# Kernel tuning notes

Hardware: AMD Instinct MI355X
Metric: run time of the kernel (lower is better)

The kernel has to match this reference:

```python
import jax, jax.numpy as jnp
import numpy as np

N = 102400          # total nodes (256 graphs x 400 nodes)
E = 3276800         # edges (avg degree 32)
B = 256             # num graphs
NODE_DIM, MRI_DIM, COG_DIM, CLIN_DIM, GEN_DIM, NUM_CLASSES = 128, 256, 64, 32, 512, 3
EPS = 1e-5

def _lin(k, i, o):
    kw, kb = jax.random.split(k)
    s = 1.0 / np.sqrt(i)
    return (jax.random.uniform(kw, (i, o), jnp.float32, -s, s),
            jax.random.uniform(kb, (o,), jnp.float32, -s, s))

def setup_inputs() -> dict:
    key = jax.random.key(0)
    ks = jax.random.split(key, 20)
    inp = {}
    inp['x'] = jax.random.normal(ks[0], (N, NODE_DIM), jnp.float32)
    inp['edge_index'] = jax.random.randint(ks[1], (2, E), 0, N)
    inp['batch'] = jnp.repeat(jnp.arange(B, dtype=jnp.int32), N // B)
    inp['mri'] = jax.random.normal(ks[2], (B, MRI_DIM), jnp.float32)
    inp['cog'] = jax.random.normal(ks[3], (B, COG_DIM), jnp.float32)
    inp['clin'] = jax.random.normal(ks[4], (B, CLIN_DIM), jnp.float32)
    inp['gen'] = jax.random.normal(ks[5], (B, GEN_DIM), jnp.float32)
    inp['W1'], inp['b1'] = _lin(ks[6], NODE_DIM, 64)
    inp['W2'], inp['b2'] = _lin(ks[7], 64, 32)
    inp['W3'], inp['b3'] = _lin(ks[8], 32, 16)
    inp['bn1_g'] = jnp.ones((64,), jnp.float32); inp['bn1_b'] = jnp.zeros((64,), jnp.float32)
    inp['bn2_g'] = jnp.ones((32,), jnp.float32); inp['bn2_b'] = jnp.zeros((32,), jnp.float32)
    inp['mriW'], inp['mrib'] = _lin(ks[9], MRI_DIM, 16)
    inp['cogW'], inp['cogb'] = _lin(ks[10], COG_DIM, 16)
    inp['clinW'], inp['clinb'] = _lin(ks[11], CLIN_DIM, 16)
    inp['genW'], inp['genb'] = _lin(ks[12], GEN_DIM, 16)
    inp['c1W'], inp['c1b'] = _lin(ks[13], 96, 64)  # 32 (pooled) + 64 (multimodal)
    inp['cbn1_g'] = jnp.ones((64,), jnp.float32); inp['cbn1_b'] = jnp.zeros((64,), jnp.float32)
    inp['c2W'], inp['c2b'] = _lin(ks[14], 64, 32)
    inp['cbn2_g'] = jnp.ones((32,), jnp.float32); inp['cbn2_b'] = jnp.zeros((32,), jnp.float32)
    inp['c3W'], inp['c3b'] = _lin(ks[15], 32, NUM_CLASSES)
    return inp

def _bn(h, g, b):
    # BatchNorm1d in training mode: biased batch stats
    m = h.mean(0)
    v = jnp.mean((h - m) ** 2, 0)
    return (h - m) * jax.lax.rsqrt(v + EPS) * g + b

def _gcn(h, W, bias, s, d, norm):
    # GCNConv: linear -> symmetric-normalized scatter-add aggregation (self-loops in s/d)
    h = h @ W
    agg = jnp.zeros_like(h).at[d].add(h[s] * norm[:, None])
    return agg + bias

def reference(x, edge_index, batch, mri, cog, clin, gen,
              W1, b1, W2, b2, W3, b3, bn1_g, bn1_b, bn2_g, bn2_b,
              mriW, mrib, cogW, cogb, clinW, clinb, genW, genb,
              c1W, c1b, cbn1_g, cbn1_b, c2W, c2b, cbn2_g, cbn2_b, c3W, c3b):
    n = x.shape[0]
    loop = jnp.arange(n)
    s = jnp.concatenate([edge_index[0], loop])
    d = jnp.concatenate([edge_index[1], loop])
    deg = jnp.zeros((n,), x.dtype).at[d].add(1.0)
    dinv = jax.lax.rsqrt(deg)  # deg >= 1 due to self-loops
    norm = dinv[s] * dinv[d]

    x1 = jax.nn.relu(_bn(_gcn(x, W1, b1, s, d, norm), bn1_g, bn1_b))
    x2 = jax.nn.relu(_bn(_gcn(x1, W2, b2, s, d, norm), bn2_g, bn2_b))
    gf = jax.nn.relu(_gcn(x2, W3, b3, s, d, norm))  # [N,16]

    cnt = jax.ops.segment_sum(jnp.ones((n,), x.dtype), batch, num_segments=B)
    g_mean = jax.ops.segment_sum(gf, batch, num_segments=B) / cnt[:, None]
    g_max = jax.ops.segment_max(gf, batch, num_segments=B)
    g_emb = jnp.concatenate([g_mean, g_max], axis=1)  # [B,32]

    mm = jnp.concatenate([
        jax.nn.relu(mri @ mriW + mrib),
        jax.nn.relu(cog @ cogW + cogb),
        jax.nn.relu(clin @ clinW + clinb),
        jax.nn.relu(gen @ genW + genb)], axis=1)  # [B,64]

    h = jnp.concatenate([g_emb, mm], axis=1)  # [B,96]
    h = jax.nn.relu(_bn(h @ c1W + c1b, cbn1_g, cbn1_b))  # dropout = identity (eval)
    h = jax.nn.relu(_bn(h @ c2W + c2b, cbn2_g, cbn2_b))
    out = h @ c3W + c3b
    return jax.nn.log_softmax(out, axis=1)
```

## Files before the change

### kernel.cpp

```cpp
#include <hip/hip_runtime.h>
#include <hip/hip_bf16.h>

#define TPB 256
#define BSHIFT 9
#define BNODES 512
#define CH 4096

typedef unsigned long long u64;
typedef __attribute__((ext_vector_type(8))) short short8;
typedef __attribute__((ext_vector_type(4))) float f32x4;

__device__ inline unsigned short f2bf(float f) {
    unsigned u = __float_as_uint(f);
    return (unsigned short)((u + 0x7FFF + ((u >> 16) & 1)) >> 16);
}
__device__ inline float bf2f(short s) {
    return __uint_as_float(((unsigned)(unsigned short)s) << 16);
}


__global__ void k_bhist(const int* __restrict__ dstp, int* __restrict__ bcnt, int E, int nbuk) {
    __shared__ int h[256];
    int tid = threadIdx.x;
    h[tid] = 0;
    __syncthreads();
    int e0 = blockIdx.x * CH;
    int e1 = min(e0 + CH, E);
    for (int e = e0 + tid; e < e1; e += TPB) atomicAdd(&h[dstp[e] >> BSHIFT], 1);
    __syncthreads();
    if (tid < nbuk && h[tid]) atomicAdd(&bcnt[tid], h[tid]);
}

__global__ void k_bscan(const int* __restrict__ bcnt, int* __restrict__ bbase,
                        int* __restrict__ gcur, int nbuk, int E) {
    __shared__ int s[256];
    int tid = threadIdx.x;
    int v = (tid < nbuk) ? bcnt[tid] : 0;
    s[tid] = v;
    __syncthreads();
    for (int o = 1; o < 256; o <<= 1) {
        int t = (tid >= o) ? s[tid - o] : 0;
        __syncthreads();
        s[tid] += t;
        __syncthreads();
    }
    if (tid < nbuk) { int e = s[tid] - v; bbase[tid] = e; gcur[tid] = e; }
    if (tid == 0) bbase[nbuk] = E;
}

__global__ void k_partition(const int* __restrict__ ei, int* __restrict__ gcur,
                            u64* __restrict__ part, int E, int nbuk) {
    __shared__ int h[256], baseg[256], scn[256], cur[256];
    __shared__ u64 stage[CH];
    int tid = threadIdx.x;
    h[tid] = 0;
    __syncthreads();
    int e0 = blockIdx.x * CH;
    int ecnt = min(CH, E - e0);
    const int* srcp = ei;
    const int* dstp = ei + E;
    for (int i = tid; i < ecnt; i += TPB) atomicAdd(&h[dstp[e0 + i] >> BSHIFT], 1);
    __syncthreads();
    int v = h[tid];
    if (tid < nbuk && v) baseg[tid] = atomicAdd(&gcur[tid], v);
    scn[tid] = v;
    __syncthreads();
    for (int o = 1; o < 256; o <<= 1) {
        int t = (tid >= o) ? scn[tid - o] : 0;
        __syncthreads();
        scn[tid] += t;
        __syncthreads();
    }
    int excl = scn[tid] - v;
    __syncthreads();
    scn[tid] = excl; cur[tid] = excl;
    __syncthreads();
    for (int i = tid; i < ecnt; i += TPB) {
        int s = srcp[e0 + i], d = dstp[e0 + i];
        int bk = d >> BSHIFT;
        int p = atomicAdd(&cur[bk], 1);
        stage[p] = ((u64)(unsigned)d << 32) | (unsigned)s;
    }
    __syncthreads();
    for (int i = tid; i < ecnt; i += TPB) {
        u64 vv = stage[i];
        int bk = (int)(vv >> 32) >> BSHIFT;
        part[baseg[bk] + (i - scn[bk])] = vv;
    }
}

__global__ void k_bucket_csr(const u64* __restrict__ part, const int* __restrict__ bbase,
                             float* __restrict__ dinv, int* __restrict__ offsets,
                             int* __restrict__ csr, int N, int nbuk) {
    __shared__ int cnt[BNODES];
    __shared__ int ps[256];
    __shared__ int off_s[BNODES];
    int b = blockIdx.x, tid = threadIdx.x;
    int n0 = b << BSHIFT;
    int nn = min(BNODES, N - n0);
    int j0 = bbase[b], j1 = bbase[b + 1];
    for (int i = tid; i < BNODES; i += TPB) cnt[i] = 0;
    __syncthreads();
    for (int j = j0 + tid; j < j1; j += TPB) {
        int dst = (int)(part[j] >> 32);
        atomicAdd(&cnt[dst - n0], 1);
    }
    __syncthreads();
    int a0 = cnt[2 * tid], a1 = cnt[2 * tid + 1];
    ps[tid] = a0 + a1;
    __syncthreads();
    for (int o = 1; o < 256; o <<= 1) {
        int t = (tid >= o) ? ps[tid - o] : 0;
        __syncthreads();
        ps[tid] += t;
        __syncthreads();
    }
    int excl = ps[tid] - (a0 + a1);
    off_s[2 * tid] = excl;
    off_s[2 * tid + 1] = excl + a0;
    __syncthreads();
    for (int i = tid; i < nn; i += TPB) {
        dinv[n0 + i] = rsqrtf((float)(cnt[i] + 1));
        offsets[n0 + i] = j0 + off_s[i];
    }
    if (b == nbuk - 1 && tid == 0) offsets[N] = j1;
    __syncthreads();
    for (int i = tid; i < BNODES; i += TPB) cnt[i] = j0 + off_s[i];
    __syncthreads();
    for (int j = j0 + tid; j < j1; j += TPB) {
        u64 vv = part[j];
        int dst = (int)(vv >> 32);
        int src = (int)(vv & 0xffffffffu);
        int pos = atomicAdd(&cnt[dst - n0], 1);
        csr[pos] = src;
    }
}


template<int K, bool BN, bool BF16IN>
__global__ void k_packA(const void* __restrict__ inv, const float* __restrict__ scale,
                        const float* __restrict__ shift, unsigned short* __restrict__ out) {
    constexpr int KB = K / 32;
    int g = blockIdx.x * TPB + threadIdx.x;
    int lane = g & 63, tile = g >> 6;
    int rowblk = tile / KB, kblk = tile - rowblk * KB;
    int row = rowblk * 16 + (lane & 15);
    int k0 = kblk * 32 + (lane >> 4) * 8;
    float vs[8];
    if (BF16IN) {
        const __hip_bfloat16* in = (const __hip_bfloat16*)inv;
        short8 sv = *reinterpret_cast<const short8*>(in + (size_t)row * K + k0);
        #pragma unroll
        for (int u = 0; u < 8; ++u) vs[u] = bf2f(sv[u]);
    } else {
        const float* in = (const float*)inv;
        const float4* p = reinterpret_cast<const float4*>(in + (size_t)row * K + k0);
        float4 v0 = p[0], v1 = p[1];
        vs[0] = v0.x; vs[1] = v0.y; vs[2] = v0.z; vs[3] = v0.w;
        vs[4] = v1.x; vs[5] = v1.y; vs[6] = v1.z; vs[7] = v1.w;
    }
    short8 rr;
    #pragma unroll
    for (int u = 0; u < 8; ++u) {
        float v = vs[u];
        if (BN) v = fmaxf(v * scale[k0 + u] + shift[k0 + u], 0.f);
        rr[u] = (short)f2bf(v);
    }
    *reinterpret_cast<short8*>(out + (size_t)g * 8) = rr;
}

__global__ void k_packW(const float* __restrict__ W1, const float* __restrict__ W2,
                        const float* __restrict__ W3, unsigned short* __restrict__ out) {
    int b = blockIdx.x, lane = threadIdx.x;
    const float* W; int KB, C; size_t off; int idx;
    if (b < 16)      { W = W1; KB = 4; C = 64; off = 0;     idx = b; }
    else if (b < 20) { W = W2; KB = 2; C = 32; off = 8192;  idx = b - 16; }
    else             { W = W3; KB = 1; C = 16; off = 10240; idx = b - 20; }
    int nblk = idx / KB, kblk = idx - nblk * KB;
    int col = nblk * 16 + (lane & 15);
    int k0 = kblk * 32 + (lane >> 4) * 8;
    short8 rr;
    #pragma unroll
    for (int j = 0; j < 8; ++j) rr[j] = (short)f2bf(W[(size_t)(k0 + j) * C + col]);
    *reinterpret_cast<short8*>(out + off + ((size_t)idx * 64 + lane) * 8) = rr;
}

template<int K, int C>
__global__ void k_mfma_gemm(const unsigned short* __restrict__ A,
                            const unsigned short* __restrict__ Wp,
                            const float* __restrict__ dinv,
                            __hip_bfloat16* __restrict__ hh, size_t slice) {
    constexpr int KB = K / 32, NB = C / 16;
    int lane = threadIdx.x & 63, w = threadIdx.x >> 6;
    int rowblk = blockIdx.x * 4 + w;
    const short8* Af = reinterpret_cast<const short8*>(A);
    const short8* Bf = reinterpret_cast<const short8*>(Wp);
    short8 b[NB][KB];
    #pragma unroll
    for (int nb = 0; nb < NB; ++nb)
        #pragma unroll
        for (int kb = 0; kb < KB; ++kb)
            b[nb][kb] = Bf[(nb * KB + kb) * 64 + lane];
    f32x4 z = {0.f, 0.f, 0.f, 0.f};
    f32x4 acc[NB];
    #pragma unroll
    for (int nb = 0; nb < NB; ++nb) acc[nb] = z;
    #pragma unroll
    for (int kb = 0; kb < KB; ++kb) {
        short8 a = Af[((size_t)rowblk * KB + kb) * 64 + lane];
        #pragma unroll
        for (int nb = 0; nb < NB; ++nb)
            acc[nb] = __builtin_amdgcn_mfma_f32_16x16x32_bf16(a, b[nb][kb], acc[nb], 0, 0, 0);
    }
    int colb = lane & 15;
    int node0 = rowblk * 16 + (lane >> 4) * 4;
    float dv[4];
    #pragma unroll
    for (int j = 0; j < 4; ++j) dv[j] = dinv[node0 + j];
    #pragma unroll
    for (int nb = 0; nb < NB; ++nb)
        #pragma unroll
        for (int j = 0; j < 4; ++j)
            hh[nb * slice + (size_t)(node0 + j) * 16 + colb] = __float2bfloat16(acc[nb][j] * dv[j]);
}

template<int CT, bool RELU, bool STATS>
__global__ void k_gather_row(const __hip_bfloat16* __restrict__ hhp,
                             const int* __restrict__ offs, const int* __restrict__ csr,
                             const float* __restrict__ dinv, const float* __restrict__ bias,
                             __hip_bfloat16* __restrict__ outp, float* __restrict__ pstat,
                             int n) {
    __shared__ float lred[16 * 272];
    __shared__ float sred[2 * 272];
    int tid = threadIdx.x;
    int g = tid >> 4, l = tid & 15;
    int node = blockIdx.x * 16 + g;
    int j0 = offs[node], j1 = offs[node + 1];
    float facc[16];
    #pragma unroll
    for (int u = 0; u < 16; ++u) facc[u] = 0.f;
    const short8* self = reinterpret_cast<const short8*>(hhp + (size_t)node * 16);
    if (l == 15) {
        short8 r0 = self[0], r1 = self[1];
        #pragma unroll
        for (int u = 0; u < 8; ++u) { facc[u] += bf2f(r0[u]); facc[8 + u] += bf2f(r1[u]); }
    }
    int j = j0 + l;
    for (; j + 16 < j1; j += 32) {
        int s0 = __builtin_nontemporal_load(&csr[j]);
        int s1 = __builtin_nontemporal_load(&csr[j + 16]);
        const short8* ra = reinterpret_cast<const short8*>(hhp + (size_t)s0 * 16);
        const short8* rb = reinterpret_cast<const short8*>(hhp + (size_t)s1 * 16);
        short8 a0 = ra[0], a1 = ra[1], b0 = rb[0], b1 = rb[1];
        #pragma unroll
        for (int u = 0; u < 8; ++u) {
            facc[u]     += bf2f(a0[u]) + bf2f(b0[u]);
            facc[8 + u] += bf2f(a1[u]) + bf2f(b1[u]);
        }
    }
    if (j < j1) {
        int s = __builtin_nontemporal_load(&csr[j]);
        const short8* row = reinterpret_cast<const short8*>(hhp + (size_t)s * 16);
        short8 r0 = row[0], r1 = row[1];
        #pragma unroll
        for (int u = 0; u < 8; ++u) { facc[u] += bf2f(r0[u]); facc[8 + u] += bf2f(r1[u]); }
    }
    int wbase = g * 272 + l * 17;
    #pragma unroll
    for (int u = 0; u < 16; ++u) lred[wbase + u] = facc[u];
    __syncthreads();
    int rbase = g * 272 + l;
    float acc = 0.f;
    #pragma unroll
    for (int k = 0; k < 16; ++k) acc += lred[rbase + k * 17];
    float v = dinv[node] * acc + bias[l];
    if (RELU) v = fmaxf(v, 0.f);
    outp[(size_t)node * CT + l] = __float2bfloat16(v);
    if (STATS) {
        sred[l * 17 + g] = v;
        sred[272 + l * 17 + g] = v * v;
        __syncthreads();
        if (tid < 32) {
            int c = tid & 15;
            const float* base = sred + (tid >> 4) * 272 + c * 17;
            float a = 0.f;
            #pragma unroll
            for (int k = 0; k < 16; ++k) a += base[k];
            pstat[(size_t)blockIdx.x * 32 + (tid >> 4) * 16 + c] = a;
        }
    }
}

__global__ void k_bnred(const float* __restrict__ pstat, float* __restrict__ bred, int G) {
    __shared__ float ss[256];
    int tid = threadIdx.x;
    int p = blockIdx.x >> 6, c = blockIdx.x & 63;
    int rows_per = (G + 63) >> 6;
    int r0 = c * rows_per, r1 = min(r0 + rows_per, G);
    const float* base = pstat + (size_t)p * G * 32;
    float acc = 0.f;
    for (int i = r0 * 32 + tid; i < r1 * 32; i += 256) acc += base[i];
    ss[tid] = acc;
    __syncthreads();
    #pragma unroll
    for (int o = 128; o >= 32; o >>= 1) {
        if (tid < o) ss[tid] += ss[tid + o];
        __syncthreads();
    }
    if (tid < 32) bred[(size_t)blockIdx.x * 32 + tid] = ss[tid];
}

__global__ void k_bnstat2(const float* __restrict__ bred, const float* __restrict__ g,
                          const float* __restrict__ b, float* __restrict__ scale,
                          float* __restrict__ shift, float invN) {
    __shared__ float ss[256];
    int tid = threadIdx.x, p = blockIdx.x;
    const float* base = bred + (size_t)p * 64 * 32;
    float acc = 0.f;
    for (int i = tid; i < 64 * 32; i += 256) acc += base[i];
    ss[tid] = acc;
    __syncthreads();
    #pragma unroll
    for (int o = 128; o >= 32; o >>= 1) {
        if (tid < o) ss[tid] += ss[tid + o];
        __syncthreads();
    }
    if (tid < 16) {
        int ch = p * 16 + tid;
        float m = ss[tid] * invN;
        float var = ss[16 + tid] * invN - m * m;
        float sc = g[ch] * rsqrtf(var + 1e-5f);
        scale[ch] = sc;
        shift[ch] = b[ch] - m * sc;
    }
}


__global__ void k_pool(const __hip_bfloat16* __restrict__ gf, float* __restrict__ h, int nper) {
    __shared__ float ssum[TPB], smax[TPB];
    int b = blockIdx.x, tid = threadIdx.x;
    int c = tid & 15, r0 = tid >> 4;
    const __hip_bfloat16* base = gf + (size_t)b * nper * 16;
    float s = 0.f, m = -1e30f;
    for (int r = r0; r < nper; r += 16) {
        float v = __bfloat162float(base[r * 16 + c]);
        s += v; m = fmaxf(m, v);
    }
    ssum[tid] = s; smax[tid] = m; __syncthreads();
    for (int off = 128; off >= 16; off >>= 1) {
        if (tid < off) { ssum[tid] += ssum[tid + off]; smax[tid] = fmaxf(smax[tid], smax[tid + off]); }
        __syncthreads();
    }
    if (tid < 16) { h[b * 96 + tid] = ssum[tid] / (float)nper; h[b * 96 + 16 + tid] = smax[tid]; }
}

__global__ void k_mm(const float* __restrict__ mri, const float* __restrict__ cog,
                     const float* __restrict__ clin, const float* __restrict__ gen,
                     const float* __restrict__ mriW, const float* __restrict__ mrib,
                     const float* __restrict__ cogW, const float* __restrict__ cogb,
                     const float* __restrict__ clinW, const float* __restrict__ clinb,
                     const float* __restrict__ genW, const float* __restrict__ genb,
                     float* __restrict__ h) {
    int b = blockIdx.x;
    int w = threadIdx.x >> 6;
    int lane = threadIdx.x & 63;
    int c = lane & 15, part = lane >> 4;
    const float* in; const float* W; const float* bias; int K;
    if (w == 0)      { in = mri  + b * 256; W = mriW;  bias = mrib;  K = 256; }
    else if (w == 1) { in = cog  + b * 64;  W = cogW;  bias = cogb;  K = 64;  }
    else if (w == 2) { in = clin + b * 32;  W = clinW; bias = clinb; K = 32;  }
    else             { in = gen  + b * 512; W = genW;  bias = genb;  K = 512; }
    int kq = K >> 2;
    int k0 = part * kq;
    float acc = 0.f;
    for (int k = k0; k < k0 + kq; k += 4) {
        float4 iv = *reinterpret_cast<const float4*>(in + k);
        acc += iv.x * W[k * 16 + c] + iv.y * W[(k + 1) * 16 + c]
             + iv.z * W[(k + 2) * 16 + c] + iv.w * W[(k + 3) * 16 + c];
    }
    acc += __shfl_xor(acc, 16);
    acc += __shfl_xor(acc, 32);
    if (part == 0) h[b * 96 + 32 + w * 16 + c] = fmaxf(acc + bias[c], 0.f);
}

__global__ void k_head1(const float* __restrict__ h, const float* __restrict__ W,
                        const float* __restrict__ bias, float* __restrict__ t1) {
    int gid = blockIdx.x * TPB + threadIdx.x;
    int b = gid >> 6, j = gid & 63;
    const float* hr = h + b * 96;
    float acc = bias[j];
    #pragma unroll
    for (int k = 0; k < 96; ++k) acc += hr[k] * W[k * 64 + j];
    t1[gid] = acc;
}

__global__ __launch_bounds__(1024) void k_headtail(
        float* __restrict__ t1g,
        const float* __restrict__ cbn1_g, const float* __restrict__ cbn1_b,
        const float* __restrict__ c2W, const float* __restrict__ c2b,
        const float* __restrict__ cbn2_g, const float* __restrict__ cbn2_b,
        const float* __restrict__ c3W, const float* __restrict__ c3b,
        float* __restrict__ out) {
    __shared__ float red[1024];
    __shared__ float t2s[256 * 32];
    __shared__ float sc1[64], sh1[64], sc2[32], sh2[32];
    int tid = threadIdx.x;
    const float invB = 1.0f / 256.0f;

    float psum = 0.f, psq = 0.f;
    for (int i = tid; i < 16384; i += 1024) {
        float v = t1g[i]; psum += v; psq += v * v;
    }
    red[tid] = psum; __syncthreads();
    for (int o = 512; o >= 64; o >>= 1) { if (tid < o) red[tid] += red[tid + o]; __syncthreads(); }
    if (tid < 64) sc1[tid] = red[tid];
    __syncthreads();
    red[tid] = psq; __syncthreads();
    for (int o = 512; o >= 64; o >>= 1) { if (tid < o) red[tid] += red[tid + o]; __syncthreads(); }
    if (tid < 64) {
        float m = sc1[tid] * invB;
        float var = red[tid] * invB - m * m;
        float s = cbn1_g[tid] * rsqrtf(var + 1e-5f);
        sc1[tid] = s; sh1[tid] = cbn1_b[tid] - m * s;
    }
    __syncthreads();
    for (int i = tid; i < 16384; i += 1024) {
        int k = i & 63;
        t1g[i] = fmaxf(t1g[i] * sc1[k] + sh1[k], 0.f);
    }
    __syncthreads();
    int j2 = tid & 31, g2 = tid >> 5;
    float p2 = 0.f, q2 = 0.f;
    for (int b = g2 * 8; b < g2 * 8 + 8; ++b) {
        const float* tr = t1g + b * 64;
        float acc = c2b[j2];
        #pragma unroll
        for (int k = 0; k < 64; ++k) acc += tr[k] * c2W[k * 32 + j2];
        t2s[b * 32 + j2] = acc; p2 += acc; q2 += acc * acc;
    }
    red[tid] = p2; __syncthreads();
    for (int o = 512; o >= 32; o >>= 1) { if (tid < o) red[tid] += red[tid + o]; __syncthreads(); }
    if (tid < 32) sc2[tid] = red[tid];
    __syncthreads();
    red[tid] = q2; __syncthreads();
    for (int o = 512; o >= 32; o >>= 1) { if (tid < o) red[tid] += red[tid + o]; __syncthreads(); }
    if (tid < 32) {
        float m = sc2[tid] * invB;
        float var = red[tid] * invB - m * m;
        float s = cbn2_g[tid] * rsqrtf(var + 1e-5f);
        sc2[tid] = s; sh2[tid] = cbn2_b[tid] - m * s;
    }
    __syncthreads();
    if (tid < 256) {
        const float* tr = t2s + tid * 32;
        float o0 = c3b[0], o1 = c3b[1], o2 = c3b[2];
        #pragma unroll
        for (int k = 0; k < 32; ++k) {
            float v = fmaxf(tr[k] * sc2[k] + sh2[k], 0.f);
            o0 += v * c3W[k * 3 + 0];
            o1 += v * c3W[k * 3 + 1];
            o2 += v * c3W[k * 3 + 2];
        }
        float m = fmaxf(fmaxf(o0, o1), o2);
        float lse = m + logf(expf(o0 - m) + expf(o1 - m) + expf(o2 - m));
        out[tid * 3 + 0] = o0 - lse;
        out[tid * 3 + 1] = o1 - lse;
        out[tid * 3 + 2] = o2 - lse;
    }
}


extern "C" void kernel_launch(void* const* d_in, const int* in_sizes, int n_in,
                              void* d_out, int out_size, void* d_ws, size_t ws_size,
                              hipStream_t stream) {
    const float* x    = (const float*)d_in[0];
    const int*   ei   = (const int*)d_in[1];
    const float* mri  = (const float*)d_in[3];
    const float* cog  = (const float*)d_in[4];
    const float* clin = (const float*)d_in[5];
    const float* gen  = (const float*)d_in[6];
    const float* W1 = (const float*)d_in[7];  const float* b1 = (const float*)d_in[8];
    const float* W2 = (const float*)d_in[9];  const float* b2 = (const float*)d_in[10];
    const float* W3 = (const float*)d_in[11]; const float* b3 = (const float*)d_in[12];
    const float* bn1_g = (const float*)d_in[13]; const float* bn1_b = (const float*)d_in[14];
    const float* bn2_g = (const float*)d_in[15]; const float* bn2_b = (const float*)d_in[16];
    const float* mriW = (const float*)d_in[17]; const float* mrib = (const float*)d_in[18];
    const float* cogW = (const float*)d_in[19]; const float* cogb = (const float*)d_in[20];
    const float* clinW = (const float*)d_in[21]; const float* clinb = (const float*)d_in[22];
    const float* genW = (const float*)d_in[23]; const float* genb = (const float*)d_in[24];
    const float* c1W = (const float*)d_in[25]; const float* c1b = (const float*)d_in[26];
    const float* cbn1_g = (const float*)d_in[27]; const float* cbn1_b = (const float*)d_in[28];
    const float* c2W = (const float*)d_in[29]; const float* c2b = (const float*)d_in[30];
    const float* cbn2_g = (const float*)d_in[31]; const float* cbn2_b = (const float*)d_in[32];
    const float* c3W = (const float*)d_in[33]; const float* c3b = (const float*)d_in[34];
    float* out = (float*)d_out;

    const int N = in_sizes[0] / 128;
    const int E = in_sizes[1] / 2;
    const int B = in_sizes[6] / 512;
    const int nper = N / B;
    const int nbuk = (N + BNODES - 1) >> BSHIFT;
    const int npart = (E + CH - 1) / CH;
    const int rowblks = N / 16;
    const int G = N / 16;

    char* ws = (char*)d_ws;
    size_t off = 0;
    auto alloc = [&](size_t bytes) -> void* {
        void* p = ws + off;
        off += (bytes + 255) & ~(size_t)255;
        return p;
    };
    int*   bcnt    = (int*)alloc(256 * 4);
    int*   bbase   = (int*)alloc((size_t)(nbuk + 1) * 4);
    int*   gcur    = (int*)alloc((size_t)nbuk * 4);
    u64*   part    = (u64*)alloc((size_t)E * 8);
    __hip_bfloat16* agg = (__hip_bfloat16*)part;
    int*   offsets = (int*)alloc((size_t)(N + 1) * 4);
    int*   csr     = (int*)alloc((size_t)E * 4);
    float* dinv    = (float*)alloc((size_t)N * 4);
    __hip_bfloat16* hh = (__hip_bfloat16*)alloc((size_t)N * 64 * 2);
    unsigned short* xb = (unsigned short*)alloc((size_t)N * 128 * 2);
    unsigned short* Wpack = (unsigned short*)alloc(10752 * 2);
    float* pstat   = (float*)alloc((size_t)6 * G * 32 * 4);
    float* bred    = (float*)alloc((size_t)6 * 64 * 32 * 4);
    float* scale1  = (float*)alloc(64 * 4);
    float* shift1  = (float*)alloc(64 * 4);
    float* scale2  = (float*)alloc(32 * 4);
    float* shift2  = (float*)alloc(32 * 4);
    float* hbuf    = (float*)alloc((size_t)B * 96 * 4);
    float* t1      = (float*)alloc((size_t)B * 64 * 4);
    (void)ws_size; (void)n_in; (void)out_size;

    hipMemsetAsync(bcnt, 0, 256 * 4, stream);

    k_bhist<<<npart, TPB, 0, stream>>>(ei + E, bcnt, E, nbuk);
    k_bscan<<<1, TPB, 0, stream>>>(bcnt, bbase, gcur, nbuk, E);
    k_partition<<<npart, TPB, 0, stream>>>(ei, gcur, part, E, nbuk);
    k_bucket_csr<<<nbuk, TPB, 0, stream>>>(part, bbase, dinv, offsets, csr, N, nbuk);
    k_packW<<<21, 64, 0, stream>>>(W1, W2, W3, Wpack);

    size_t slice = (size_t)N * 16;
    int gmm = rowblks / 4;

    k_packA<128, false, false><<<rowblks * 4 * 64 / TPB, TPB, 0, stream>>>(x, nullptr, nullptr, xb);
    k_mfma_gemm<128, 64><<<gmm, TPB, 0, stream>>>(xb, Wpack, dinv, hh, slice);
    for (int p = 0; p < 4; ++p)
        k_gather_row<64, false, true><<<G, TPB, 0, stream>>>(
            hh + p * slice, offsets, csr, dinv, b1 + p * 16,
            agg + p * 16, pstat + (size_t)p * G * 32, N);
    k_bnred<<<4 * 64, 256, 0, stream>>>(pstat, bred, G);
    k_bnstat2<<<4, 256, 0, stream>>>(bred, bn1_g, bn1_b, scale1, shift1, 1.0f / N);

    k_packA<64, true, true><<<rowblks * 2 * 64 / TPB, TPB, 0, stream>>>(agg, scale1, shift1, xb);
    k_mfma_gemm<64, 32><<<gmm, TPB, 0, stream>>>(xb, Wpack + 8192, dinv, hh, slice);
    for (int p = 0; p < 2; ++p)
        k_gather_row<32, false, true><<<G, TPB, 0, stream>>>(
            hh + p * slice, offsets, csr, dinv, b2 + p * 16,
            agg + p * 16, pstat + (size_t)(4 + p) * G * 32, N);
    k_bnred<<<2 * 64, 256, 0, stream>>>(pstat + (size_t)4 * G * 32, bred + 4 * 64 * 32, G);
    k_bnstat2<<<2, 256, 0, stream>>>(bred + 4 * 64 * 32, bn2_g, bn2_b, scale2, shift2, 1.0f / N);

    k_packA<32, true, true><<<rowblks * 1 * 64 / TPB, TPB, 0, stream>>>(agg, scale2, shift2, xb);
    k_mfma_gemm<32, 16><<<gmm, TPB, 0, stream>>>(xb, Wpack + 10240, dinv, hh, slice);
    k_gather_row<16, true, false><<<G, TPB, 0, stream>>>(hh, offsets, csr, dinv, b3, agg, nullptr, N);

    k_pool<<<B, TPB, 0, stream>>>(agg, hbuf, nper);
    k_mm<<<B, 256, 0, stream>>>(mri, cog, clin, gen, mriW, mrib, cogW, cogb,
                                clinW, clinb, genW, genb, hbuf);
    k_head1<<<(B * 64 + TPB - 1) / TPB, TPB, 0, stream>>>(hbuf, c1W, c1b, t1);
    k_headtail<<<1, 1024, 0, stream>>>(t1, cbn1_g, cbn1_b, c2W, c2b,
                                       cbn2_g, cbn2_b, c3W, c3b, out);
}
```

Baseline: 418.3 us.

## Gather 32-channel slices per pass to halve CSR traversals in GCN layers

The GEMM epilogue now writes features in 32-channel slices instead of 16, and a new gather kernel accumulates 32 channels per edge visit, so layer 1 takes two gather passes instead of four and layer 2 takes one instead of two. This cuts repeated reads of the CSR index array and the per-pass launch overhead, while each random row fetch becomes 64 bytes. The BN partial-stat reductions are resized to 64 entries per block, and the per-thread accumulator doubles to 32 floats, which raises register pressure. The bucket CSR build also switches its reads of the partitioned edge array to nontemporal loads.

New measurement: 408.1 us. -2.4%, faster.

```diff
diff --git a/kernel.cpp b/kernel.cpp
--- a/kernel.cpp
+++ b/kernel.cpp
@@ -102,8 +102,8 @@
     for (int i = tid; i < BNODES; i += TPB) cnt[i] = 0;
     __syncthreads();
     for (int j = j0 + tid; j < j1; j += TPB) {
-        int dst = (int)(part[j] >> 32);
-        atomicAdd(&cnt[dst - n0], 1);
+        u64 vv = __builtin_nontemporal_load(&part[j]);
+        atomicAdd(&cnt[(int)(vv >> 32) - n0], 1);
     }
     __syncthreads();
     int a0 = cnt[2 * tid], a1 = cnt[2 * tid + 1];
@@ -128,7 +128,7 @@
     for (int i = tid; i < BNODES; i += TPB) cnt[i] = j0 + off_s[i];
     __syncthreads();
     for (int j = j0 + tid; j < j1; j += TPB) {
-        u64 vv = part[j];
+        u64 vv = __builtin_nontemporal_load(&part[j]);
         int dst = (int)(vv >> 32);
         int src = (int)(vv & 0xffffffffu);
         int pos = atomicAdd(&cnt[dst - n0], 1);
@@ -185,7 +185,7 @@
     *reinterpret_cast<short8*>(out + off + ((size_t)idx * 64 + lane) * 8) = rr;
 }
 
-template<int K, int C>
+template<int K, int C, int SW>
 __global__ void k_mfma_gemm(const unsigned short* __restrict__ A,
                             const unsigned short* __restrict__ Wp,
                             const float* __restrict__ dinv,
@@ -218,20 +218,105 @@
     #pragma unroll
     for (int j = 0; j < 4; ++j) dv[j] = dinv[node0 + j];
     #pragma unroll
-    for (int nb = 0; nb < NB; ++nb)
+    for (int nb = 0; nb < NB; ++nb) {
+        int c = nb * 16 + colb;
+        size_t base = (size_t)(c / SW) * slice + (c % SW);
         #pragma unroll
         for (int j = 0; j < 4; ++j)
-            hh[nb * slice + (size_t)(node0 + j) * 16 + colb] = __float2bfloat16(acc[nb][j] * dv[j]);
+            hh[base + (size_t)(node0 + j) * SW] = __float2bfloat16(acc[nb][j] * dv[j]);
+    }
 }
 
 template<int CT, bool RELU, bool STATS>
+__global__ void k_gather_row32(const __hip_bfloat16* __restrict__ hhp,
+                               const int* __restrict__ offs, const int* __restrict__ csr,
+                               const float* __restrict__ dinv, const float* __restrict__ bias,
+                               __hip_bfloat16* __restrict__ outp, float* __restrict__ pstat,
+                               int n) {
+    __shared__ float lred[16 * 528];
+    __shared__ float sred[2 * 544];
+    int tid = threadIdx.x;
+    int g = tid >> 4, l = tid & 15;
+    int node = blockIdx.x * 16 + g;
+    int j0 = offs[node], j1 = offs[node + 1];
+    float facc[32];
+    #pragma unroll
+    for (int u = 0; u < 32; ++u) facc[u] = 0.f;
+    if (l == 15) {
+        const short8* sr = reinterpret_cast<const short8*>(hhp + (size_t)node * 32);
+        short8 r0 = sr[0], r1 = sr[1], r2 = sr[2], r3 = sr[3];
+        #pragma unroll
+        for (int u = 0; u < 8; ++u) {
+            facc[u] += bf2f(r0[u]);      facc[8 + u]  += bf2f(r1[u]);
+            facc[16 + u] += bf2f(r2[u]); facc[24 + u] += bf2f(r3[u]);
+        }
+    }
+    int j = j0 + l;
+    for (; j + 16 < j1; j += 32) {
+        int s0 = __builtin_nontemporal_load(&csr[j]);
+        int s1 = __builtin_nontemporal_load(&csr[j + 16]);
+        const short8* ra = reinterpret_cast<const short8*>(hhp + (size_t)s0 * 32);
+        const short8* rb = reinterpret_cast<const short8*>(hhp + (size_t)s1 * 32);
+        short8 a0 = ra[0], a1 = ra[1], a2 = ra[2], a3 = ra[3];
+        short8 b0 = rb[0], b1 = rb[1], b2 = rb[2], b3 = rb[3];
+        #pragma unroll
+        for (int u = 0; u < 8; ++u) {
+            facc[u]      += bf2f(a0[u]) + bf2f(b0[u]);
+            facc[8 + u]  += bf2f(a1[u]) + bf2f(b1[u]);
+            facc[16 + u] += bf2f(a2[u]) + bf2f(b2[u]);
+            facc[24 + u] += bf2f(a3[u]) + bf2f(b3[u]);
+        }
+    }
+    if (j < j1) {
+        int s = __builtin_nontemporal_load(&csr[j]);
+        const short8* rr = reinterpret_cast<const short8*>(hhp + (size_t)s * 32);
+        short8 r0 = rr[0], r1 = rr[1], r2 = rr[2], r3 = rr[3];
+        #pragma unroll
+        for (int u = 0; u < 8; ++u) {
+            facc[u] += bf2f(r0[u]);      facc[8 + u]  += bf2f(r1[u]);
+            facc[16 + u] += bf2f(r2[u]); facc[24 + u] += bf2f(r3[u]);
+        }
+    }
+    int wbase = g * 528 + l * 33;
+    #pragma unroll
+    for (int u = 0; u < 32; ++u) lred[wbase + u] = facc[u];
+    __syncthreads();
+    int rbase = g * 528 + l;
+    float alo = 0.f, ahi = 0.f;
+    #pragma unroll
+    for (int k = 0; k < 16; ++k) {
+        alo += lred[rbase + k * 33];
+        ahi += lred[rbase + k * 33 + 16];
+    }
+    float dv = dinv[node];
+    float vlo = dv * alo + bias[l];
+    float vhi = dv * ahi + bias[l + 16];
+    if (RELU) { vlo = fmaxf(vlo, 0.f); vhi = fmaxf(vhi, 0.f); }
+    outp[(size_t)node * CT + l]      = __float2bfloat16(vlo);
+    outp[(size_t)node * CT + l + 16] = __float2bfloat16(vhi);
+    if (STATS) {
+        sred[l * 17 + g]          = vlo;
+        sred[(l + 16) * 17 + g]   = vhi;
+        sred[544 + l * 17 + g]        = vlo * vlo;
+        sred[544 + (l + 16) * 17 + g] = vhi * vhi;
+        __syncthreads();
+        if (tid < 64) {
+            int which = tid >> 5, c = tid & 31;
+            const float* base = sred + which * 544 + c * 17;
+            float a = 0.f;
+            #pragma unroll
+            for (int k = 0; k < 16; ++k) a += base[k];
+            pstat[(size_t)blockIdx.x * 64 + which * 32 + c] = a;
+        }
+    }
+}
+
+template<int CT, bool RELU>
 __global__ void k_gather_row(const __hip_bfloat16* __restrict__ hhp,
                              const int* __restrict__ offs, const int* __restrict__ csr,
                              const float* __restrict__ dinv, const float* __restrict__ bias,
-                             __hip_bfloat16* __restrict__ outp, float* __restrict__ pstat,
-                             int n) {
+                             __hip_bfloat16* __restrict__ outp, int n) {
     __shared__ float lred[16 * 272];
-    __shared__ float sred[2 * 272];
     int tid = threadIdx.x;
     int g = tid >> 4, l = tid & 15;
     int node = blockIdx.x * 16 + g;
@@ -239,9 +324,9 @@
     float facc[16];
     #pragma unroll
     for (int u = 0; u < 16; ++u) facc[u] = 0.f;
-    const short8* self = reinterpret_cast<const short8*>(hhp + (size_t)node * 16);
     if (l == 15) {
-        short8 r0 = self[0], r1 = self[1];
+        const short8* sr = reinterpret_cast<const short8*>(hhp + (size_t)node * 16);
+        short8 r0 = sr[0], r1 = sr[1];
         #pragma unroll
         for (int u = 0; u < 8; ++u) { facc[u] += bf2f(r0[u]); facc[8 + u] += bf2f(r1[u]); }
     }
@@ -260,8 +345,8 @@
     }
     if (j < j1) {
         int s = __builtin_nontemporal_load(&csr[j]);
-        const short8* row = reinterpret_cast<const short8*>(hhp + (size_t)s * 16);
-        short8 r0 = row[0], r1 = row[1];
+        const short8* rr = reinterpret_cast<const short8*>(hhp + (size_t)s * 16);
+        short8 r0 = rr[0], r1 = rr[1];
         #pragma unroll
         for (int u = 0; u < 8; ++u) { facc[u] += bf2f(r0[u]); facc[8 + u] += bf2f(r1[u]); }
     }
@@ -276,19 +361,6 @@
     float v = dinv[node] * acc + bias[l];
     if (RELU) v = fmaxf(v, 0.f);
     outp[(size_t)node * CT + l] = __float2bfloat16(v);
-    if (STATS) {
-        sred[l * 17 + g] = v;
-        sred[272 + l * 17 + g] = v * v;
-        __syncthreads();
-        if (tid < 32) {
-            int c = tid & 15;
-            const float* base = sred + (tid >> 4) * 272 + c * 17;
-            float a = 0.f;
-            #pragma unroll
-            for (int k = 0; k < 16; ++k) a += base[k];
-            pstat[(size_t)blockIdx.x * 32 + (tid >> 4) * 16 + c] = a;
-        }
-    }
 }
 
 __global__ void k_bnred(const float* __restrict__ pstat, float* __restrict__ bred, int G) {
@@ -297,17 +369,17 @@
     int p = blockIdx.x >> 6, c = blockIdx.x & 63;
     int rows_per = (G + 63) >> 6;
     int r0 = c * rows_per, r1 = min(r0 + rows_per, G);
-    const float* base = pstat + (size_t)p * G * 32;
+    const float* base = pstat + (size_t)p * G * 64;
     float acc = 0.f;
-    for (int i = r0 * 32 + tid; i < r1 * 32; i += 256) acc += base[i];
+    for (int i = r0 * 64 + tid; i < r1 * 64; i += 256) acc += base[i];
     ss[tid] = acc;
     __syncthreads();
     #pragma unroll
-    for (int o = 128; o >= 32; o >>= 1) {
+    for (int o = 128; o >= 64; o >>= 1) {
         if (tid < o) ss[tid] += ss[tid + o];
         __syncthreads();
     }
-    if (tid < 32) bred[(size_t)blockIdx.x * 32 + tid] = ss[tid];
+    if (tid < 64) bred[(size_t)blockIdx.x * 64 + tid] = ss[tid];
 }
 
 __global__ void k_bnstat2(const float* __restrict__ bred, const float* __restrict__ g,
@@ -315,20 +387,20 @@
                           float* __restrict__ shift, float invN) {
     __shared__ float ss[256];
     int tid = threadIdx.x, p = blockIdx.x;
-    const float* base = bred + (size_t)p * 64 * 32;
+    const float* base = bred + (size_t)p * 64 * 64;
     float acc = 0.f;
-    for (int i = tid; i < 64 * 32; i += 256) acc += base[i];
+    for (int i = tid; i < 64 * 64; i += 256) acc += base[i];
     ss[tid] = acc;
     __syncthreads();
     #pragma unroll
-    for (int o = 128; o >= 32; o >>= 1) {
+    for (int o = 128; o >= 64; o >>= 1) {
         if (tid < o) ss[tid] += ss[tid + o];
         __syncthreads();
     }
-    if (tid < 16) {
-        int ch = p * 16 + tid;
+    if (tid < 32) {
+        int ch = p * 32 + tid;
         float m = ss[tid] * invN;
-        float var = ss[16 + tid] * invN - m * m;
+        float var = ss[32 + tid] * invN - m * m;
         float sc = g[ch] * rsqrtf(var + 1e-5f);
         scale[ch] = sc;
         shift[ch] = b[ch] - m * sc;
@@ -522,8 +594,8 @@
     __hip_bfloat16* hh = (__hip_bfloat16*)alloc((size_t)N * 64 * 2);
     unsigned short* xb = (unsigned short*)alloc((size_t)N * 128 * 2);
     unsigned short* Wpack = (unsigned short*)alloc(10752 * 2);
-    float* pstat   = (float*)alloc((size_t)6 * G * 32 * 4);
-    float* bred    = (float*)alloc((size_t)6 * 64 * 32 * 4);
+    float* pstat   = (float*)alloc((size_t)3 * G * 64 * 4);
+    float* bred    = (float*)alloc((size_t)3 * 64 * 64 * 4);
     float* scale1  = (float*)alloc(64 * 4);
     float* shift1  = (float*)alloc(64 * 4);
     float* scale2  = (float*)alloc(32 * 4);
@@ -540,30 +612,28 @@
     k_bucket_csr<<<nbuk, TPB, 0, stream>>>(part, bbase, dinv, offsets, csr, N, nbuk);
     k_packW<<<21, 64, 0, stream>>>(W1, W2, W3, Wpack);
 
-    size_t slice = (size_t)N * 16;
+    size_t slice32 = (size_t)N * 32;
     int gmm = rowblks / 4;
 
     k_packA<128, false, false><<<rowblks * 4 * 64 / TPB, TPB, 0, stream>>>(x, nullptr, nullptr, xb);
-    k_mfma_gemm<128, 64><<<gmm, TPB, 0, stream>>>(xb, Wpack, dinv, hh, slice);
-    for (int p = 0; p < 4; ++p)
-        k_gather_row<64, false, true><<<G, TPB, 0, stream>>>(
-            hh + p * slice, offsets, csr, dinv, b1 + p * 16,
-            agg + p * 16, pstat + (size_t)p * G * 32, N);
-    k_bnred<<<4 * 64, 256, 0, stream>>>(pstat, bred, G);
-    k_bnstat2<<<4, 256, 0, stream>>>(bred, bn1_g, bn1_b, scale1, shift1, 1.0f / N);
+    k_mfma_gemm<128, 64, 32><<<gmm, TPB, 0, stream>>>(xb, Wpack, dinv, hh, slice32);
+    for (int p = 0; p < 2; ++p)
+        k_gather_row32<64, false, true><<<G, TPB, 0, stream>>>(
+            hh + p * slice32, offsets, csr, dinv, b1 + p * 32,
+            agg + p * 32, pstat + (size_t)p * G * 64, N);
+    k_bnred<<<2 * 64, 256, 0, stream>>>(pstat, bred, G);
+    k_bnstat2<<<2, 256, 0, stream>>>(bred, bn1_g, bn1_b, scale1, shift1, 1.0f / N);
 
     k_packA<64, true, true><<<rowblks * 2 * 64 / TPB, TPB, 0, stream>>>(agg, scale1, shift1, xb);
-    k_mfma_gemm<64, 32><<<gmm, TPB, 0, stream>>>(xb, Wpack + 8192, dinv, hh, slice);
-    for (int p = 0; p < 2; ++p)
-        k_gather_row<32, false, true><<<G, TPB, 0, stream>>>(
-            hh + p * slice, offsets, csr, dinv, b2 + p * 16,
-            agg + p * 16, pstat + (size_t)(4 + p) * G * 32, N);
-    k_bnred<<<2 * 64, 256, 0, stream>>>(pstat + (size_t)4 * G * 32, bred + 4 * 64 * 32, G);
-    k_bnstat2<<<2, 256, 0, stream>>>(bred + 4 * 64 * 32, bn2_g, bn2_b, scale2, shift2, 1.0f / N);
+    k_mfma_gemm<64, 32, 32><<<gmm, TPB, 0, stream>>>(xb, Wpack + 8192, dinv, hh, slice32);
+    k_gather_row32<32, false, true><<<G, TPB, 0, stream>>>(
+        hh, offsets, csr, dinv, b2, agg, pstat + (size_t)2 * G * 64, N);
+    k_bnred<<<64, 256, 0, stream>>>(pstat + (size_t)2 * G * 64, bred + 2 * 64 * 64, G);
+    k_bnstat2<<<1, 256, 0, stream>>>(bred + 2 * 64 * 64, bn2_g, bn2_b, scale2, shift2, 1.0f / N);
 
     k_packA<32, true, true><<<rowblks * 1 * 64 / TPB, TPB, 0, stream>>>(agg, scale2, shift2, xb);
-    k_mfma_gemm<32, 16><<<gmm, TPB, 0, stream>>>(xb, Wpack + 10240, dinv, hh, slice);
-    k_gather_row<16, true, false><<<G, TPB, 0, stream>>>(hh, offsets, csr, dinv, b3, agg, nullptr, N);
+    k_mfma_gemm<32, 16, 16><<<gmm, TPB, 0, stream>>>(xb, Wpack + 10240, dinv, hh, (size_t)N * 16);
+    k_gather_row<16, true><<<G, TPB, 0, stream>>>(hh, offsets, csr, dinv, b3, agg, N);
 
     k_pool<<<B, TPB, 0, stream>>>(agg, hbuf, nper);
     k_mm<<<B, 256, 0, stream>>>(mri, cog, clin, gen, mriW, mrib, cogW, cogb,
```
